# Kernel optimization log

Hardware: AMD Instinct MI355X
Metric: run time of the kernel (lower is better)

## Reference

```python
import jax, jax.numpy as jnp
import numpy as np

N_NODES = 100000
N_EDGES = 600000
IN_DIM = 128
OUT_DIM = 64


def setup_inputs() -> dict:
    key = jax.random.key(0)
    k1, k2, k3, k4, k5 = jax.random.split(key, 5)
    x = jax.random.normal(k1, (N_NODES, IN_DIM), dtype=jnp.float32)
    edge_index = jax.random.randint(k2, (2, N_EDGES), 0, N_NODES, dtype=jnp.int64)
    edge_weight = jax.random.uniform(k3, (N_EDGES,), dtype=jnp.float32)
    W1 = jax.random.normal(k4, (IN_DIM, IN_DIM), dtype=jnp.float32) / np.sqrt(IN_DIM)
    b1 = jnp.zeros((IN_DIM,), dtype=jnp.float32)
    W2 = jax.random.normal(k5, (IN_DIM, OUT_DIM), dtype=jnp.float32) / np.sqrt(IN_DIM)
    b2 = jnp.zeros((OUT_DIM,), dtype=jnp.float32)
    return {"x": x, "edge_index": edge_index, "edge_weight": edge_weight,
            "W1": W1, "b1": b1, "W2": W2, "b2": b2}


def _spmm(edge_index, edge_weight, h):
    # out[dst] = sum_{e: dst(e)=dst} w_e * h[src(e)]  -- normalized adjacency SpMM
    src, dst = edge_index[0], edge_index[1]
    msg = h[src] * edge_weight[:, None]          # [E, D] gather + scale
    return jax.ops.segment_sum(msg, dst, num_segments=h.shape[0])  # [N, D]


def reference(x, edge_index, edge_weight, W1, b1, W2, b2):
    # Layer 1: GCNConv(in,in) -> ReLU (dropout is identity in eval mode)
    h = _spmm(edge_index, edge_weight, x @ W1) + b1
    h = jax.nn.relu(h)
    # Layer 2: GCNConv(in,out)
    out = _spmm(edge_index, edge_weight, h @ W2) + b2
    return out
```

## Files before the change

kernel.cpp:

```cpp
#include <hip/hip_runtime.h>

#define NN 100000
#define NE 600000
#define DIN 128
#define DOUT 64
#define SCAN_B 256
#define NBLK ((NN + SCAN_B - 1) / SCAN_B)
#define HIST_B ((NE + 255) / 256)
#define PREP_N (DIN * DIN + DIN * DOUT)
#define PREP_B ((PREP_N + 255) / 256)

typedef __attribute__((ext_vector_type(8))) short bf16x8;
typedef __attribute__((ext_vector_type(4))) short s16x4;
typedef __attribute__((ext_vector_type(4))) float f32x4;

__device__ inline short f2bf(float f) {
  union { float f; unsigned u; } v; v.f = f;
  unsigned r = (v.u + 0x7FFF + ((v.u >> 16) & 1)) >> 16;
  return (short)r;
}
__device__ inline float bf2f(unsigned short u) {
  union { unsigned u; float f; } v; v.u = ((unsigned)u) << 16;
  return v.f;
}

__global__ __launch_bounds__(256) void hist_prep_kernel(const int* __restrict__ ei,
                                                        int* __restrict__ cnt,
                                                        const float* __restrict__ W1,
                                                        short* __restrict__ w1t,
                                                        const float* __restrict__ W2,
                                                        short* __restrict__ w2t) {
  const int b = blockIdx.x, t = threadIdx.x;
  if (b < HIST_B) {
    int e = b * 256 + t;
    if (e < NE) atomicAdd(&cnt[ei[NE + e]], 1);
  } else {
    int i = (b - HIST_B) * 256 + t;
    if (i < DIN * DIN) {
      int n = i >> 7, k = i & 127;
      w1t[i] = f2bf(W1[k * DIN + n]);
    } else if (i < PREP_N) {
      int i2 = i - DIN * DIN;
      int n = i2 >> 7, k = i2 & 127;
      w2t[i2] = f2bf(W2[k * DOUT + n]);
    }
  }
}

__global__ __launch_bounds__(256) void scan_local_kernel(const int* __restrict__ cnt,
                                                         int* __restrict__ row_ptr,
                                                         int* __restrict__ blk_sum) {
  __shared__ int s[256];
  const int b = blockIdx.x, t = threadIdx.x;
  const int i = b * 256 + t;
  int v = (i < NN) ? cnt[i] : 0;
  s[t] = v;
  __syncthreads();
  for (int off = 1; off < 256; off <<= 1) {
    int u = (t >= off) ? s[t - off] : 0;
    __syncthreads();
    s[t] += u;
    __syncthreads();
  }
  if (i < NN) row_ptr[i] = s[t] - v;
  if (t == 255) blk_sum[b] = s[255];
}

__global__ __launch_bounds__(512) void scan_blk_kernel(const int* __restrict__ blk_sum,
                                                       int* __restrict__ blk_off) {
  __shared__ int s[512];
  const int t = threadIdx.x;
  int v = (t < NBLK) ? blk_sum[t] : 0;
  s[t] = v;
  __syncthreads();
  for (int off = 1; off < 512; off <<= 1) {
    int u = (t >= off) ? s[t - off] : 0;
    __syncthreads();
    s[t] += u;
    __syncthreads();
  }
  if (t < NBLK) blk_off[t] = s[t] - v;
}

__global__ __launch_bounds__(256) void scan_add_kernel(int* __restrict__ row_ptr,
                                                       const int* __restrict__ blk_off,
                                                       int* __restrict__ next) {
  const int b = blockIdx.x, t = threadIdx.x;
  const int i = b * 256 + t;
  if (i < NN) {
    int v = row_ptr[i] + blk_off[b];
    row_ptr[i] = v;
    next[i] = v;
  }
  if (i == 0) row_ptr[NN] = NE;
}

__global__ __launch_bounds__(256) void scatter_kernel(const int* __restrict__ ei,
                                                      const float* __restrict__ ew,
                                                      int* __restrict__ next,
                                                      int* __restrict__ col,
                                                      float* __restrict__ wv) {
  int e = blockIdx.x * 256 + threadIdx.x;
  if (e >= NE) return;
  int src = ei[e];
  int dst = ei[NE + e];
  int pos = atomicAdd(&next[dst], 1);
  col[pos] = src;
  wv[pos] = ew[e];
}

#define G1_BM 128
#define XS_PITCH 136
__global__ __launch_bounds__(256) void gemm1_mfma_kernel(const float* __restrict__ x,
                                                         const short* __restrict__ w1t,
                                                         short* __restrict__ h0) {
  __shared__ short xs[G1_BM][XS_PITCH];
  const int t = threadIdx.x;
  const int row0 = blockIdx.x * G1_BM;
#pragma unroll
  for (int i = 0; i < 16; ++i) {
    int f = t + i * 256;
    int r = f >> 5, c4 = f & 31;
    int gr = row0 + r;
    float4 v = (gr < NN) ? *(const float4*)&x[(size_t)gr * DIN + c4 * 4]
                         : make_float4(0.f, 0.f, 0.f, 0.f);
    s16x4 s;
    s.x = f2bf(v.x); s.y = f2bf(v.y); s.z = f2bf(v.z); s.w = f2bf(v.w);
    *(s16x4*)&xs[r][c4 * 4] = s;
  }
  __syncthreads();

  const int wave = t >> 6, lane = t & 63;
  const int nlane = lane & 15, quad = lane >> 4;
  const int mbase = wave * 32;
  f32x4 acc[2][8];
#pragma unroll
  for (int mt = 0; mt < 2; ++mt)
#pragma unroll
    for (int nt = 0; nt < 8; ++nt) acc[mt][nt] = (f32x4){0.f, 0.f, 0.f, 0.f};

#pragma unroll
  for (int ks = 0; ks < 4; ++ks) {
    const int koff = ks * 32 + quad * 8;
    bf16x8 a0 = *(const bf16x8*)&xs[mbase + nlane][koff];
    bf16x8 a1 = *(const bf16x8*)&xs[mbase + 16 + nlane][koff];
#pragma unroll
    for (int nt = 0; nt < 8; ++nt) {
      bf16x8 b = *(const bf16x8*)&w1t[(size_t)(nt * 16 + nlane) * DIN + koff];
      acc[0][nt] = __builtin_amdgcn_mfma_f32_16x16x32_bf16(a0, b, acc[0][nt], 0, 0, 0);
      acc[1][nt] = __builtin_amdgcn_mfma_f32_16x16x32_bf16(a1, b, acc[1][nt], 0, 0, 0);
    }
  }

#pragma unroll
  for (int mt = 0; mt < 2; ++mt)
#pragma unroll
    for (int nt = 0; nt < 8; ++nt)
#pragma unroll
      for (int rg = 0; rg < 4; ++rg) {
        int gr = row0 + mbase + mt * 16 + quad * 4 + rg;
        if (gr < NN) h0[(size_t)gr * DIN + nt * 16 + nlane] = f2bf(acc[mt][nt][rg]);
      }
}

__global__ __launch_bounds__(256) void gemm2_mfma_kernel(const float* __restrict__ acc1,
                                                         const float* __restrict__ b1,
                                                         const short* __restrict__ w2t,
                                                         short* __restrict__ h2) {
  __shared__ short xs[G1_BM][XS_PITCH];
  const int t = threadIdx.x;
  const int row0 = blockIdx.x * G1_BM;
#pragma unroll
  for (int i = 0; i < 16; ++i) {
    int f = t + i * 256;
    int r = f >> 5, c4 = f & 31;
    int gr = row0 + r;
    float4 v = (gr < NN) ? *(const float4*)&acc1[(size_t)gr * DIN + c4 * 4]
                         : make_float4(0.f, 0.f, 0.f, 0.f);
    float4 bb = *(const float4*)&b1[c4 * 4];
    s16x4 s;
    s.x = f2bf(fmaxf(v.x + bb.x, 0.f));
    s.y = f2bf(fmaxf(v.y + bb.y, 0.f));
    s.z = f2bf(fmaxf(v.z + bb.z, 0.f));
    s.w = f2bf(fmaxf(v.w + bb.w, 0.f));
    *(s16x4*)&xs[r][c4 * 4] = s;
  }
  __syncthreads();

  const int wave = t >> 6, lane = t & 63;
  const int nlane = lane & 15, quad = lane >> 4;
  const int mbase = wave * 32;
  f32x4 acc[2][4];
#pragma unroll
  for (int mt = 0; mt < 2; ++mt)
#pragma unroll
    for (int nt = 0; nt < 4; ++nt) acc[mt][nt] = (f32x4){0.f, 0.f, 0.f, 0.f};

#pragma unroll
  for (int ks = 0; ks < 4; ++ks) {
    const int koff = ks * 32 + quad * 8;
    bf16x8 a0 = *(const bf16x8*)&xs[mbase + nlane][koff];
    bf16x8 a1 = *(const bf16x8*)&xs[mbase + 16 + nlane][koff];
#pragma unroll
    for (int nt = 0; nt < 4; ++nt) {
      bf16x8 b = *(const bf16x8*)&w2t[(size_t)(nt * 16 + nlane) * DIN + koff];
      acc[0][nt] = __builtin_amdgcn_mfma_f32_16x16x32_bf16(a0, b, acc[0][nt], 0, 0, 0);
      acc[1][nt] = __builtin_amdgcn_mfma_f32_16x16x32_bf16(a1, b, acc[1][nt], 0, 0, 0);
    }
  }

#pragma unroll
  for (int mt = 0; mt < 2; ++mt)
#pragma unroll
    for (int nt = 0; nt < 4; ++nt)
#pragma unroll
      for (int rg = 0; rg < 4; ++rg) {
        int gr = row0 + mbase + mt * 16 + quad * 4 + rg;
        if (gr < NN) h2[(size_t)gr * DOUT + nt * 16 + nlane] = f2bf(acc[mt][nt][rg]);
      }
}

template <int D, int LPE, bool BIAS>
__global__ __launch_bounds__(256) void spmm_gather_bf16_kernel(
    const int* __restrict__ rp, const int* __restrict__ col,
    const float* __restrict__ wv, const short* __restrict__ h,
    const float* __restrict__ bias, float* __restrict__ out) {
  const int row = blockIdx.x * (256 / LPE) + threadIdx.x / LPE;
  const int lane = threadIdx.x % LPE;
  if (row >= NN) return;
  const int b = rp[row], e = rp[row + 1];
  float acc[8];
#pragma unroll
  for (int j = 0; j < 8; ++j) acc[j] = 0.f;
  int i = b;
  for (; i + 2 <= e; i += 2) {
    int s0 = col[i], s1 = col[i + 1];
    float w0 = wv[i], w1 = wv[i + 1];
    bf16x8 v0 = *(const bf16x8*)&h[(size_t)s0 * D + lane * 8];
    bf16x8 v1 = *(const bf16x8*)&h[(size_t)s1 * D + lane * 8];
#pragma unroll
    for (int j = 0; j < 8; ++j)
      acc[j] += w0 * bf2f((unsigned short)v0[j]) + w1 * bf2f((unsigned short)v1[j]);
  }
  if (i < e) {
    int s0 = col[i];
    float w0 = wv[i];
    bf16x8 v0 = *(const bf16x8*)&h[(size_t)s0 * D + lane * 8];
#pragma unroll
    for (int j = 0; j < 8; ++j) acc[j] += w0 * bf2f((unsigned short)v0[j]);
  }
  if (BIAS) {
#pragma unroll
    for (int j = 0; j < 8; ++j) acc[j] += bias[lane * 8 + j];
  }
  float4 o0 = make_float4(acc[0], acc[1], acc[2], acc[3]);
  float4 o1 = make_float4(acc[4], acc[5], acc[6], acc[7]);
  *(float4*)&out[(size_t)row * D + lane * 8] = o0;
  *(float4*)&out[(size_t)row * D + lane * 8 + 4] = o1;
}

extern "C" void kernel_launch(void* const* d_in, const int* in_sizes, int n_in,
                              void* d_out, int out_size, void* d_ws, size_t ws_size,
                              hipStream_t stream) {
  const float* x  = (const float*)d_in[0];
  const int*   ei = (const int*)d_in[1];
  const float* ew = (const float*)d_in[2];
  const float* W1 = (const float*)d_in[3];
  const float* b1 = (const float*)d_in[4];
  const float* W2 = (const float*)d_in[5];
  const float* b2 = (const float*)d_in[6];
  float* out = (float*)d_out;

  char* p = (char*)d_ws;
  int*   cnt     = (int*)p;                 p += sizeof(int) * NN;
  int*   row_ptr = (int*)p;                 p += sizeof(int) * (NN + 4);
  int*   blk_sum = (int*)p;                 p += sizeof(int) * (NBLK + 1);
  int*   blk_off = (int*)p;                 p += sizeof(int) * (NBLK + 1);
  int*   col     = (int*)p;                 p += sizeof(int) * NE;
  float* wv      = (float*)p;               p += sizeof(float) * NE;
  short* w1t     = (short*)p;               p += sizeof(short) * DIN * DIN;
  short* w2t     = (short*)p;               p += sizeof(short) * DIN * DOUT;
  short* h0      = (short*)p;               p += sizeof(short) * (size_t)NN * DIN;
  float* acc1    = (float*)p;
  int*   next    = cnt;
  short* h2      = h0;

  hipMemsetAsync(cnt, 0, sizeof(int) * NN, stream);
  hist_prep_kernel<<<HIST_B + PREP_B, 256, 0, stream>>>(ei, cnt, W1, w1t, W2, w2t);
  scan_local_kernel<<<NBLK, 256, 0, stream>>>(cnt, row_ptr, blk_sum);
  scan_blk_kernel<<<1, 512, 0, stream>>>(blk_sum, blk_off);
  scan_add_kernel<<<NBLK, 256, 0, stream>>>(row_ptr, blk_off, next);
  scatter_kernel<<<HIST_B, 256, 0, stream>>>(ei, ew, next, col, wv);

  gemm1_mfma_kernel<<<(NN + G1_BM - 1) / G1_BM, 256, 0, stream>>>(x, w1t, h0);
  spmm_gather_bf16_kernel<DIN, 16, false>
      <<<(NN * 16 + 255) / 256, 256, 0, stream>>>(row_ptr, col, wv, h0, nullptr, acc1);

  gemm2_mfma_kernel<<<(NN + G1_BM - 1) / G1_BM, 256, 0, stream>>>(acc1, b1, w2t, h2);
  spmm_gather_bf16_kernel<DOUT, 8, true>
      <<<(NN * 8 + 255) / 256, 256, 0, stream>>>(row_ptr, col, wv, h2, b2, out);
}
```

Before: 276.5 us.

## Pack edge col/weight pairs, store SpMM intermediate in bf16, unroll gather by four

The scatter now writes each CSR entry as one packed int2 (source index plus weight bits) instead of two separate arrays, so the gather reads one 8-byte entry per edge. The first SpMM writes its output in bf16 instead of fp32, which halves the intermediate traffic between SpMM1 and GEMM2. The gather loop is also unrolled to four edges so more independent row loads are in flight. Rounding the pre-ReLU sums to bf16 adds some numerical error.

After: 261.7 us. -5.4%, faster.

```diff
diff --git a/kernel.cpp b/kernel.cpp
--- a/kernel.cpp
+++ b/kernel.cpp
@@ -98,15 +98,13 @@
 __global__ __launch_bounds__(256) void scatter_kernel(const int* __restrict__ ei,
                                                       const float* __restrict__ ew,
                                                       int* __restrict__ next,
-                                                      int* __restrict__ col,
-                                                      float* __restrict__ wv) {
+                                                      int2* __restrict__ ep) {
   int e = blockIdx.x * 256 + threadIdx.x;
   if (e >= NE) return;
   int src = ei[e];
   int dst = ei[NE + e];
   int pos = atomicAdd(&next[dst], 1);
-  col[pos] = src;
-  wv[pos] = ew[e];
+  ep[pos] = make_int2(src, __float_as_int(ew[e]));
 }
 
 #define G1_BM 128
@@ -163,7 +161,7 @@
       }
 }
 
-__global__ __launch_bounds__(256) void gemm2_mfma_kernel(const float* __restrict__ acc1,
+__global__ __launch_bounds__(256) void gemm2_mfma_kernel(const short* __restrict__ acc1,
                                                          const float* __restrict__ b1,
                                                          const short* __restrict__ w2t,
                                                          short* __restrict__ h2) {
@@ -171,19 +169,19 @@
   const int t = threadIdx.x;
   const int row0 = blockIdx.x * G1_BM;
 #pragma unroll
-  for (int i = 0; i < 16; ++i) {
+  for (int i = 0; i < 8; ++i) {
     int f = t + i * 256;
-    int r = f >> 5, c4 = f & 31;
+    int r = f >> 4, c8 = f & 15;
     int gr = row0 + r;
-    float4 v = (gr < NN) ? *(const float4*)&acc1[(size_t)gr * DIN + c4 * 4]
-                         : make_float4(0.f, 0.f, 0.f, 0.f);
-    float4 bb = *(const float4*)&b1[c4 * 4];
-    s16x4 s;
-    s.x = f2bf(fmaxf(v.x + bb.x, 0.f));
-    s.y = f2bf(fmaxf(v.y + bb.y, 0.f));
-    s.z = f2bf(fmaxf(v.z + bb.z, 0.f));
-    s.w = f2bf(fmaxf(v.w + bb.w, 0.f));
-    *(s16x4*)&xs[r][c4 * 4] = s;
+    bf16x8 v = (gr < NN) ? *(const bf16x8*)&acc1[(size_t)gr * DIN + c8 * 8]
+                         : (bf16x8){0, 0, 0, 0, 0, 0, 0, 0};
+    bf16x8 s;
+#pragma unroll
+    for (int j = 0; j < 8; ++j) {
+      float fv = bf2f((unsigned short)v[j]) + b1[c8 * 8 + j];
+      s[j] = f2bf(fmaxf(fv, 0.f));
+    }
+    *(bf16x8*)&xs[r][c8 * 8] = s;
   }
   __syncthreads();
 
@@ -220,11 +218,11 @@
       }
 }
 
-template <int D, int LPE, bool BIAS>
-__global__ __launch_bounds__(256) void spmm_gather_bf16_kernel(
-    const int* __restrict__ rp, const int* __restrict__ col,
-    const float* __restrict__ wv, const short* __restrict__ h,
-    const float* __restrict__ bias, float* __restrict__ out) {
+template <int D, int LPE, bool BIAS, bool OUTBF>
+__global__ __launch_bounds__(256) void spmm_gather_kernel(
+    const int* __restrict__ rp, const int2* __restrict__ ep,
+    const short* __restrict__ h, const float* __restrict__ bias,
+    void* __restrict__ outv) {
   const int row = blockIdx.x * (256 / LPE) + threadIdx.x / LPE;
   const int lane = threadIdx.x % LPE;
   if (row >= NN) return;
@@ -233,19 +231,33 @@
 #pragma unroll
   for (int j = 0; j < 8; ++j) acc[j] = 0.f;
   int i = b;
-  for (; i + 2 <= e; i += 2) {
-    int s0 = col[i], s1 = col[i + 1];
-    float w0 = wv[i], w1 = wv[i + 1];
-    bf16x8 v0 = *(const bf16x8*)&h[(size_t)s0 * D + lane * 8];
-    bf16x8 v1 = *(const bf16x8*)&h[(size_t)s1 * D + lane * 8];
+  for (; i + 4 <= e; i += 4) {
+    int2 p0 = ep[i], p1 = ep[i + 1], p2 = ep[i + 2], p3 = ep[i + 3];
+    bf16x8 v0 = *(const bf16x8*)&h[(size_t)p0.x * D + lane * 8];
+    bf16x8 v1 = *(const bf16x8*)&h[(size_t)p1.x * D + lane * 8];
+    bf16x8 v2 = *(const bf16x8*)&h[(size_t)p2.x * D + lane * 8];
+    bf16x8 v3 = *(const bf16x8*)&h[(size_t)p3.x * D + lane * 8];
+    float w0 = __int_as_float(p0.y), w1 = __int_as_float(p1.y);
+    float w2 = __int_as_float(p2.y), w3 = __int_as_float(p3.y);
+#pragma unroll
+    for (int j = 0; j < 8; ++j)
+      acc[j] += w0 * bf2f((unsigned short)v0[j]) + w1 * bf2f((unsigned short)v1[j]) +
+                w2 * bf2f((unsigned short)v2[j]) + w3 * bf2f((unsigned short)v3[j]);
+  }
+  if (i + 2 <= e) {
+    int2 p0 = ep[i], p1 = ep[i + 1];
+    bf16x8 v0 = *(const bf16x8*)&h[(size_t)p0.x * D + lane * 8];
+    bf16x8 v1 = *(const bf16x8*)&h[(size_t)p1.x * D + lane * 8];
+    float w0 = __int_as_float(p0.y), w1 = __int_as_float(p1.y);
 #pragma unroll
     for (int j = 0; j < 8; ++j)
       acc[j] += w0 * bf2f((unsigned short)v0[j]) + w1 * bf2f((unsigned short)v1[j]);
+    i += 2;
   }
   if (i < e) {
-    int s0 = col[i];
-    float w0 = wv[i];
-    bf16x8 v0 = *(const bf16x8*)&h[(size_t)s0 * D + lane * 8];
+    int2 p0 = ep[i];
+    bf16x8 v0 = *(const bf16x8*)&h[(size_t)p0.x * D + lane * 8];
+    float w0 = __int_as_float(p0.y);
 #pragma unroll
     for (int j = 0; j < 8; ++j) acc[j] += w0 * bf2f((unsigned short)v0[j]);
   }
@@ -253,10 +265,16 @@
 #pragma unroll
     for (int j = 0; j < 8; ++j) acc[j] += bias[lane * 8 + j];
   }
-  float4 o0 = make_float4(acc[0], acc[1], acc[2], acc[3]);
-  float4 o1 = make_float4(acc[4], acc[5], acc[6], acc[7]);
-  *(float4*)&out[(size_t)row * D + lane * 8] = o0;
-  *(float4*)&out[(size_t)row * D + lane * 8 + 4] = o1;
+  if (OUTBF) {
+    bf16x8 o;
+#pragma unroll
+    for (int j = 0; j < 8; ++j) o[j] = f2bf(acc[j]);
+    *(bf16x8*)((short*)outv + (size_t)row * D + lane * 8) = o;
+  } else {
+    float* out = (float*)outv;
+    *(float4*)&out[(size_t)row * D + lane * 8] = make_float4(acc[0], acc[1], acc[2], acc[3]);
+    *(float4*)&out[(size_t)row * D + lane * 8 + 4] = make_float4(acc[4], acc[5], acc[6], acc[7]);
+  }
 }
 
 extern "C" void kernel_launch(void* const* d_in, const int* in_sizes, int n_in,
@@ -276,12 +294,11 @@
   int*   row_ptr = (int*)p;                 p += sizeof(int) * (NN + 4);
   int*   blk_sum = (int*)p;                 p += sizeof(int) * (NBLK + 1);
   int*   blk_off = (int*)p;                 p += sizeof(int) * (NBLK + 1);
-  int*   col     = (int*)p;                 p += sizeof(int) * NE;
-  float* wv      = (float*)p;               p += sizeof(float) * NE;
+  int2*  ep      = (int2*)p;                p += sizeof(int2) * NE;
   short* w1t     = (short*)p;               p += sizeof(short) * DIN * DIN;
   short* w2t     = (short*)p;               p += sizeof(short) * DIN * DOUT;
   short* h0      = (short*)p;               p += sizeof(short) * (size_t)NN * DIN;
-  float* acc1    = (float*)p;
+  short* acc1    = (short*)p;
   int*   next    = cnt;
   short* h2      = h0;
 
@@ -290,13 +307,13 @@
   scan_local_kernel<<<NBLK, 256, 0, stream>>>(cnt, row_ptr, blk_sum);
   scan_blk_kernel<<<1, 512, 0, stream>>>(blk_sum, blk_off);
   scan_add_kernel<<<NBLK, 256, 0, stream>>>(row_ptr, blk_off, next);
-  scatter_kernel<<<HIST_B, 256, 0, stream>>>(ei, ew, next, col, wv);
+  scatter_kernel<<<HIST_B, 256, 0, stream>>>(ei, ew, next, ep);
 
   gemm1_mfma_kernel<<<(NN + G1_BM - 1) / G1_BM, 256, 0, stream>>>(x, w1t, h0);
-  spmm_gather_bf16_kernel<DIN, 16, false>
-      <<<(NN * 16 + 255) / 256, 256, 0, stream>>>(row_ptr, col, wv, h0, nullptr, acc1);
+  spmm_gather_kernel<DIN, 16, false, true>
+      <<<(NN * 16 + 255) / 256, 256, 0, stream>>>(row_ptr, ep, h0, nullptr, acc1);
 
   gemm2_mfma_kernel<<<(NN + G1_BM - 1) / G1_BM, 256, 0, stream>>>(acc1, b1, w2t, h2);
-  spmm_gather_bf16_kernel<DOUT, 8, true>
-      <<<(NN * 8 + 255) / 256, 256, 0, stream>>>(row_ptr, col, wv, h2, b2, out);
-}
+  spmm_gather_kernel<DOUT, 8, true, false>
+      <<<(NN * 8 + 255) / 256, 256, 0, stream>>>(row_ptr, ep, h2, b2, out);
+}
```
